# Kernel tuning notes

Hardware: AMD Instinct MI355X
Metric: run time of the kernel (lower is better)

Reference implementation:

```python
import jax, jax.numpy as jnp
import numpy as np

# Probabilistic Conway forward prop: for each cell, let p_i be the live
# probability of its 8 Moore neighbors (torus wrap via roll). The output is
# P(exactly 3 live neighbors) + P(exactly 2 live neighbors) * p_self.
# The original enumerates all C(8,2)=28 and C(8,3)=56 combinations of
# degree-8 products; here we compute the identical Poisson-binomial pmf
# values with the standard DP recurrence pmf_k <- pmf_k*(1-p) + pmf_{k-1}*p,
# truncated at k=3 (truncation does not affect pmf_2 / pmf_3).

MOORE_OFFSETS = [(i, j) for i in (-1, 0, 1) for j in (-1, 0, 1) if (i, j) != (0, 0)]


def setup_inputs() -> dict:
    key = jax.random.key(0)
    inputs = jax.random.uniform(key, (32, 1024, 1024), dtype=jnp.float32)
    return {"inputs": inputs}


def reference(inputs):
    pmf0 = jnp.ones_like(inputs)
    pmf1 = jnp.zeros_like(inputs)
    pmf2 = jnp.zeros_like(inputs)
    pmf3 = jnp.zeros_like(inputs)
    for shift in MOORE_OFFSETS:  # fixed 8-iteration stencil loop
        p = jnp.roll(inputs, shift, axis=(-2, -1))
        q = 1.0 - p
        pmf3 = pmf3 * q + pmf2 * p
        pmf2 = pmf2 * q + pmf1 * p
        pmf1 = pmf1 * q + pmf0 * p
        pmf0 = pmf0 * q
    # P(live next) = P(3 live nbrs) + P(2 live nbrs) * P(self live)
    return pmf3 + pmf2 * inputs
```

## Files before the change

kernel.cpp:

```cpp
#include <hip/hip_runtime.h>


#define H 1024
#define W 1024
#define RPT 8
#define NROWS (RPT + 2)

__global__ __launch_bounds__(256) void prob_conway_kernel(
    const float* __restrict__ in, float* __restrict__ out) {
    const int nblk = 32 * (H / RPT);
    const int cpx  = nblk / 8;
    const int bid  = blockIdx.x;
    const int s    = (bid & 7) * cpx + (bid >> 3);

    const int plane = s >> 7;
    const int rg    = s & 127;
    const int r0    = rg * RPT;
    const int lane  = threadIdx.x & 63;
    const int c0    = threadIdx.x * 4;

    const float* __restrict__ img = in + (size_t)plane * (H * W);
    float* __restrict__ o         = out + (size_t)plane * (H * W);

    float P[NROWS][6];
#pragma unroll
    for (int i = 0; i < NROWS; ++i) {
        const int r = (r0 + i - 1 + H) & (H - 1);
        const float4 v = *reinterpret_cast<const float4*>(img + (size_t)r * W + c0);
        P[i][1] = v.x; P[i][2] = v.y; P[i][3] = v.z; P[i][4] = v.w;
    }

    const int wbase = (threadIdx.x >> 6) << 8;
    const int clw   = (wbase + W - 1) & (W - 1);
    const int crw   = (wbase + 256) & (W - 1);
    int gi = lane >> 1;
    gi = (gi < NROWS) ? gi : 0;
    const int grow = (r0 + gi - 1 + H) & (H - 1);
    const int gcol = (lane & 1) ? crw : clw;
    const float gv = img[(size_t)grow * W + gcol];

#pragma unroll
    for (int i = 0; i < NROWS; ++i) {
        const float lv = __shfl_up(P[i][4], 1);
        const float rv = __shfl_down(P[i][1], 1);
        const float e  = __shfl(gv, 2 * i + ((lane == 63) ? 1 : 0));
        P[i][0] = (lane == 0)  ? e : lv;
        P[i][5] = (lane == 63) ? e : rv;
    }

#pragma unroll
    for (int j = 0; j < RPT; ++j) {
        float res[4];
#pragma unroll
        for (int x = 0; x < 4; ++x) {
            const float nbr[8] = {
                P[j][x],     P[j][x + 1],     P[j][x + 2],
                P[j + 1][x],                  P[j + 1][x + 2],
                P[j + 2][x], P[j + 2][x + 1], P[j + 2][x + 2]
            };
            float pmf0 = 1.0f, pmf1 = 0.0f, pmf2 = 0.0f, pmf3 = 0.0f;
#pragma unroll
            for (int k = 0; k < 8; ++k) {
                const float pv = nbr[k];
                const float qv = 1.0f - pv;
                pmf3 = pmf3 * qv + pmf2 * pv;
                pmf2 = pmf2 * qv + pmf1 * pv;
                pmf1 = pmf1 * qv + pmf0 * pv;
                pmf0 = pmf0 * qv;
            }
            res[x] = pmf3 + pmf2 * P[j + 1][x + 1];
        }
        float4 rv4;
        rv4.x = res[0]; rv4.y = res[1]; rv4.z = res[2]; rv4.w = res[3];
        *reinterpret_cast<float4*>(o + (size_t)(r0 + j) * W + c0) = rv4;
    }
}

extern "C" void kernel_launch(void* const* d_in, const int* in_sizes, int n_in,
                              void* d_out, int out_size, void* d_ws, size_t ws_size,
                              hipStream_t stream) {
    const float* in = (const float*)d_in[0];
    float* out = (float*)d_out;
    dim3 grid(32 * (H / RPT));
    dim3 block(256);
    prob_conway_kernel<<<grid, block, 0, stream>>>(in, out);
}
```

Measured before the change: 53.91 us.

## Share per-column 3-cell pmf partials across adjacent outputs via convolution

Rather than running the 8-step Poisson-binomial recurrence for every output pixel, each column's vertical triple gets its pmf computed once and reused. Left and right columns (3 cells each) and the middle column's top/bottom pair (2 cells) are then combined with small truncated convolutions. This removes redundant arithmetic across the four adjacent outputs each thread produces. The cost is more live registers and a slightly different floating-point summation order.

```diff
diff --git a/kernel.cpp b/kernel.cpp
--- a/kernel.cpp
+++ b/kernel.cpp
@@ -50,24 +50,37 @@
 
 #pragma unroll
     for (int j = 0; j < RPT; ++j) {
+        float v3[6][4];
+        float dd[4][3];
+#pragma unroll
+        for (int jc = 0; jc < 6; ++jc) {
+            const float a  = P[j][jc];
+            const float b  = P[j + 1][jc];
+            const float cc = P[j + 2][jc];
+            const float qa = 1.0f - a, qb = 1.0f - b, qc = 1.0f - cc;
+            const float d0 = qa * qc;
+            const float d1 = qa * cc + a * qc;
+            const float d2 = a * cc;
+            v3[jc][0] = d0 * qb;
+            v3[jc][1] = d1 * qb + d0 * b;
+            v3[jc][2] = d2 * qb + d1 * b;
+            v3[jc][3] = d2 * b;
+            if (jc >= 1 && jc <= 4) {
+                dd[jc - 1][0] = d0; dd[jc - 1][1] = d1; dd[jc - 1][2] = d2;
+            }
+        }
         float res[4];
 #pragma unroll
         for (int x = 0; x < 4; ++x) {
-            const float nbr[8] = {
-                P[j][x],     P[j][x + 1],     P[j][x + 2],
-                P[j + 1][x],                  P[j + 1][x + 2],
-                P[j + 2][x], P[j + 2][x + 1], P[j + 2][x + 2]
-            };
-            float pmf0 = 1.0f, pmf1 = 0.0f, pmf2 = 0.0f, pmf3 = 0.0f;
-#pragma unroll
-            for (int k = 0; k < 8; ++k) {
-                const float pv = nbr[k];
-                const float qv = 1.0f - pv;
-                pmf3 = pmf3 * qv + pmf2 * pv;
-                pmf2 = pmf2 * qv + pmf1 * pv;
-                pmf1 = pmf1 * qv + pmf0 * pv;
-                pmf0 = pmf0 * qv;
-            }
+            const float* L = v3[x];
+            const float* R = v3[x + 2];
+            const float* D = dd[x];
+            const float w0 = L[0] * R[0];
+            const float w1 = L[1] * R[0] + L[0] * R[1];
+            const float w2 = L[2] * R[0] + L[1] * R[1] + L[0] * R[2];
+            const float w3 = L[3] * R[0] + L[2] * R[1] + L[1] * R[2] + L[0] * R[3];
+            const float pmf2 = w2 * D[0] + w1 * D[1] + w0 * D[2];
+            const float pmf3 = w3 * D[0] + w2 * D[1] + w1 * D[2];
             res[x] = pmf3 + pmf2 * P[j + 1][x + 1];
         }
         float4 rv4;
```

New measurement: 52.00 us. -3.5%, faster.

## Factor neighbor pmf via column triplet convolution with packed float2 math and larger row tiles

Applied to the files above, without the earlier changes.

Rewrites the per-cell Poisson-binomial DP as a separable convolution. Per-column pmfs of the vertical triplet are computed once and shared across adjacent output cells, then combined with the middle column's pair pmf. The math uses float2 vectors so the compiler can emit packed FP32 ops. Rows per block go from 8 to 16, cutting halo reloads, and loads are staged in phases to overlap with compute. Stores become nontemporal. The cost is higher register pressure and a different floating-point summation order.

```diff
diff --git a/kernel.cpp b/kernel.cpp
--- a/kernel.cpp
+++ b/kernel.cpp
@@ -3,77 +3,134 @@
 
 #define H 1024
 #define W 1024
-#define RPT 8
-#define NROWS (RPT + 2)
+#define RPB 16
+#define NR (RPB + 2)
+
+typedef float f32x4 __attribute__((ext_vector_type(4)));
+typedef float f32x2 __attribute__((ext_vector_type(2)));
 
 __global__ __launch_bounds__(256) void prob_conway_kernel(
     const float* __restrict__ in, float* __restrict__ out) {
-    const int nblk = 32 * (H / RPT);
+    const int nblk = 32 * (H / RPB);
     const int cpx  = nblk / 8;
     const int bid  = blockIdx.x;
     const int s    = (bid & 7) * cpx + (bid >> 3);
 
-    const int plane = s >> 7;
-    const int rg    = s & 127;
-    const int r0    = rg * RPT;
+    const int plane = s >> 6;
+    const int rg    = s & 63;
+    const int r0    = rg * RPB;
     const int lane  = threadIdx.x & 63;
     const int c0    = threadIdx.x * 4;
 
     const float* __restrict__ img = in + (size_t)plane * (H * W);
     float* __restrict__ o         = out + (size_t)plane * (H * W);
 
-    float P[NROWS][6];
-#pragma unroll
-    for (int i = 0; i < NROWS; ++i) {
-        const int r = (r0 + i - 1 + H) & (H - 1);
-        const float4 v = *reinterpret_cast<const float4*>(img + (size_t)r * W + c0);
-        P[i][1] = v.x; P[i][2] = v.y; P[i][3] = v.z; P[i][4] = v.w;
-    }
-
     const int wbase = (threadIdx.x >> 6) << 8;
     const int clw   = (wbase + W - 1) & (W - 1);
     const int crw   = (wbase + 256) & (W - 1);
     int gi = lane >> 1;
-    gi = (gi < NROWS) ? gi : 0;
+    gi = (gi < NR) ? gi : 0;
     const int grow = (r0 + gi - 1 + H) & (H - 1);
     const int gcol = (lane & 1) ? crw : clw;
     const float gv = img[(size_t)grow * W + gcol];
 
-#pragma unroll
-    for (int i = 0; i < NROWS; ++i) {
-        const float lv = __shfl_up(P[i][4], 1);
-        const float rv = __shfl_down(P[i][1], 1);
-        const float e  = __shfl(gv, 2 * i + ((lane == 63) ? 1 : 0));
-        P[i][0] = (lane == 0)  ? e : lv;
-        P[i][5] = (lane == 63) ? e : rv;
+    float P[NR][6];
+
+#define LOADROW(i)                                                         \
+    {                                                                      \
+        const int r = (r0 + (i) - 1 + H) & (H - 1);                        \
+        const f32x4 v =                                                    \
+            *reinterpret_cast<const f32x4*>(img + (size_t)r * W + c0);     \
+        P[i][1] = v.x; P[i][2] = v.y; P[i][3] = v.z; P[i][4] = v.w;        \
     }
 
-#pragma unroll
-    for (int j = 0; j < RPT; ++j) {
-        float res[4];
-#pragma unroll
-        for (int x = 0; x < 4; ++x) {
-            const float nbr[8] = {
-                P[j][x],     P[j][x + 1],     P[j][x + 2],
-                P[j + 1][x],                  P[j + 1][x + 2],
-                P[j + 2][x], P[j + 2][x + 1], P[j + 2][x + 2]
-            };
-            float pmf0 = 1.0f, pmf1 = 0.0f, pmf2 = 0.0f, pmf3 = 0.0f;
-#pragma unroll
-            for (int k = 0; k < 8; ++k) {
-                const float pv = nbr[k];
-                const float qv = 1.0f - pv;
-                pmf3 = pmf3 * qv + pmf2 * pv;
-                pmf2 = pmf2 * qv + pmf1 * pv;
-                pmf1 = pmf1 * qv + pmf0 * pv;
-                pmf0 = pmf0 * qv;
-            }
-            res[x] = pmf3 + pmf2 * P[j + 1][x + 1];
-        }
-        float4 rv4;
-        rv4.x = res[0]; rv4.y = res[1]; rv4.z = res[2]; rv4.w = res[3];
-        *reinterpret_cast<float4*>(o + (size_t)(r0 + j) * W + c0) = rv4;
+#define HALO(i)                                                            \
+    {                                                                      \
+        const float lv = __shfl_up(P[i][4], 1);                            \
+        const float rv = __shfl_down(P[i][1], 1);                          \
+        const float e  = __shfl(gv, 2 * (i) + ((lane == 63) ? 1 : 0));     \
+        P[i][0] = (lane == 0)  ? e : lv;                                   \
+        P[i][5] = (lane == 63) ? e : rv;                                   \
     }
+
+#define PHASE(pbase, obase)                                                \
+    {                                                                      \
+        f32x2 Q[6][6];                                                     \
+        _Pragma("unroll")                                                  \
+        for (int i = 0; i < 4; ++i)                                        \
+            _Pragma("unroll")                                              \
+            for (int c = 0; c < 6; ++c)                                    \
+                Q[i][c] = f32x2{P[(pbase) + i][c], P[(pbase) + i + 2][c]}; \
+        _Pragma("unroll")                                                  \
+        for (int k = 0; k < 2; ++k) {                                      \
+            f32x2 v3[6][4];                                                \
+            f32x2 dd[4][3];                                                \
+            _Pragma("unroll")                                              \
+            for (int jc = 0; jc < 6; ++jc) {                               \
+                const f32x2 a  = Q[k][jc];                                 \
+                const f32x2 b  = Q[k + 1][jc];                             \
+                const f32x2 cc = Q[k + 2][jc];                             \
+                const f32x2 qa = 1.0f - a, qb = 1.0f - b, qc = 1.0f - cc;  \
+                const f32x2 d0 = qa * qc;                                  \
+                const f32x2 d1 = qa * cc + a * qc;                         \
+                const f32x2 d2 = a * cc;                                   \
+                v3[jc][0] = d0 * qb;                                       \
+                v3[jc][1] = d1 * qb + d0 * b;                              \
+                v3[jc][2] = d2 * qb + d1 * b;                              \
+                v3[jc][3] = d2 * b;                                        \
+                if (jc >= 1 && jc <= 4) {                                  \
+                    dd[jc - 1][0] = d0; dd[jc - 1][1] = d1;                \
+                    dd[jc - 1][2] = d2;                                    \
+                }                                                          \
+            }                                                              \
+            f32x2 res[4];                                                  \
+            _Pragma("unroll")                                              \
+            for (int x = 0; x < 4; ++x) {                                  \
+                const f32x2* L = v3[x];                                    \
+                const f32x2* R = v3[x + 2];                                \
+                const f32x2* D = dd[x];                                    \
+                const f32x2 w0 = L[0] * R[0];                              \
+                const f32x2 w1 = L[1] * R[0] + L[0] * R[1];                \
+                const f32x2 w2 = L[2] * R[0] + L[1] * R[1] + L[0] * R[2];  \
+                const f32x2 w3 = L[3] * R[0] + L[2] * R[1] + L[1] * R[2]   \
+                               + L[0] * R[3];                              \
+                const f32x2 pmf2 = w2 * D[0] + w1 * D[1] + w0 * D[2];      \
+                const f32x2 pmf3 = w3 * D[0] + w2 * D[1] + w1 * D[2];      \
+                res[x] = pmf3 + pmf2 * Q[k + 1][x + 1];                    \
+            }                                                              \
+            const f32x4 lo = {res[0].x, res[1].x, res[2].x, res[3].x};     \
+            const f32x4 hi = {res[0].y, res[1].y, res[2].y, res[3].y};     \
+            __builtin_nontemporal_store(lo,                                \
+                reinterpret_cast<f32x4*>(                                  \
+                    o + (size_t)((obase) + k) * W + c0));                  \
+            __builtin_nontemporal_store(hi,                                \
+                reinterpret_cast<f32x4*>(                                  \
+                    o + (size_t)((obase) + k + 2) * W + c0));              \
+        }                                                                  \
+    }
+
+    LOADROW(0) LOADROW(1) LOADROW(2) LOADROW(3) LOADROW(4)
+    LOADROW(5) LOADROW(6) LOADROW(7) LOADROW(8) LOADROW(9)
+
+    HALO(0) HALO(1) HALO(2) HALO(3) HALO(4) HALO(5)
+    PHASE(0, r0)
+
+    LOADROW(10) LOADROW(11) LOADROW(12) LOADROW(13)
+
+    HALO(6) HALO(7) HALO(8) HALO(9)
+    PHASE(4, r0 + 4)
+
+    LOADROW(14) LOADROW(15) LOADROW(16) LOADROW(17)
+
+    HALO(10) HALO(11) HALO(12) HALO(13)
+    PHASE(8, r0 + 8)
+
+    HALO(14) HALO(15) HALO(16) HALO(17)
+    PHASE(12, r0 + 12)
+
+#undef LOADROW
+#undef HALO
+#undef PHASE
 }
 
 extern "C" void kernel_launch(void* const* d_in, const int* in_sizes, int n_in,
@@ -81,7 +138,7 @@
                               hipStream_t stream) {
     const float* in = (const float*)d_in[0];
     float* out = (float*)d_out;
-    dim3 grid(32 * (H / RPT));
+    dim3 grid(32 * (H / RPB));
     dim3 block(256);
     prob_conway_kernel<<<grid, block, 0, stream>>>(in, out);
 }
```

Result: faster. 46.99 us (-12.8%).
